# Optimization experiments

Measured on AMD Instinct MI355X. Metric: run time of the kernel, lower is better.

## Reference

```python
import jax, jax.numpy as jnp
import numpy as np

M = 150000  # number of nodes
K = 64      # neighbor_limits[-1]


def setup_inputs() -> dict:
    key = jax.random.key(0)
    k1, k2 = jax.random.split(key)
    nodes = jax.random.normal(k1, (M, 3), dtype=jnp.float32)
    # radius_search-style neighbor table: values in [0, M], where index == M is padding
    node_knn_indices = jax.random.randint(k2, (M, K), 0, M + 1, dtype=jnp.int64)
    return {"nodes": nodes, "node_knn_indices": node_knn_indices}


def _greedy_nms(knn):
    # Sequential greedy suppression: node i is kept iff none of its radius
    # neighbors with smaller index was already kept. masks has size M+1 so the
    # padding index M always reads False (never suppresses).
    m = knn.shape[0]
    masks0 = jnp.zeros(m + 1, dtype=bool)

    def step(masks, xs):
        i, row = xs
        keep = ~jnp.any(masks[row])  # masks[node_knn_indices[i]].sum() == 0
        return masks.at[i].set(keep), None

    masks, _ = jax.lax.scan(step, masks0, (jnp.arange(m), knn))
    return masks


def reference(nodes, node_knn_indices):
    masks = _greedy_nms(node_knn_indices)
    kept = masks[:-1]  # [M] bool
    # Original returns node_knn_indices[kept] (data-dependent shape). For a
    # jit-compatible fixed shape we return the full table with suppressed rows
    # overwritten by the padding index M; kept rows are bitwise identical.
    m = node_knn_indices.shape[0]
    kept_knn = jnp.where(kept[:, None], node_knn_indices, m)
    return kept, kept_knn
```

## Files before the change

### kernel.cpp

```cpp
#include <hip/hip_runtime.h>


#define M_ROWS 150000
#define KNN    64
#define BLK    1024
#define QRT    2
#define CHUNK  (BLK * QRT)
#define NCH    ((M_ROWS + CHUNK - 1) / CHUNK)
#define ICAP   6
#define ECAP   16
#define WCH    8
#define W64PC  (CHUNK / 32)
#define LMW    (((NCH - 1) * CHUNK) / 32)
#define NBMG   ((NCH - 1) * W64PC)
#define OUT_INTS (M_ROWS + M_ROWS * KNN)
#define BMG_INT_OFF (OUT_INTS - NBMG * 2)
#define VALIDB (1ull << 32)

__global__ void init_ws_kernel(unsigned int* progress, int* out) {
  const int i = blockIdx.x * blockDim.x + threadIdx.x;
  unsigned long long* bmg64 = (unsigned long long*)(out + BMG_INT_OFF);
  if (i < NBMG) bmg64[i] = 0ull;
  if (i == 0) *progress = 0u;
}

__device__ __forceinline__ bool probe_reload(const int* __restrict__ rp,
                                             const unsigned int* lm,
                                             int lo, int hi) {
  bool s = false;
#pragma unroll
  for (int u = 0; u < 16; ++u) {
    int4 d = ((const int4*)rp)[u];
    int js[4] = {d.x, d.y, d.z, d.w};
#pragma unroll
    for (int m = 0; m < 4; ++m) {
      int j = js[m];
      if (j >= lo && j < hi && ((lm[j >> 5] >> (j & 31)) & 1u)) s = true;
    }
  }
  return s;
}

__global__ __launch_bounds__(BLK) void nms_chain_kernel(
    const int* __restrict__ knn,
    int* __restrict__ out,
    unsigned int* __restrict__ progress)
{
  const int b    = blockIdx.x;
  const int t    = threadIdx.x;
  const int base = b * CHUNK;
  const int winb = (b > WCH) ? (base - WCH * CHUNK) : 0;

  unsigned long long* bmg64 = (unsigned long long*)(out + BMG_INT_OFF);

  __shared__ unsigned char      st[CHUNK];
  __shared__ unsigned short     il[ICAP][CHUNK];
  __shared__ unsigned short     exl[ECAP][CHUNK];
  __shared__ unsigned int       lm[LMW];
  __shared__ unsigned int       sh_p;

  int  rowq[QRT];
  bool vq[QRT], ovf[QRT], eovf[QRT], supp[QRT];
  int  ic[QRT], ec[QRT];

#pragma unroll
  for (int q = 0; q < QRT; ++q) {
    rowq[q] = base + q * BLK + t;
    vq[q]   = rowq[q] < M_ROWS;
    ic[q] = ec[q] = 0;
    ovf[q] = eovf[q] = supp[q] = false;
  }

#pragma unroll
  for (int q = 0; q < QRT; ++q) {
    if (!vq[q]) continue;
    const int o   = q * BLK + t;
    const int row = rowq[q];
    const int* rp = knn + (long long)row * KNN;
#pragma unroll
    for (int u = 0; u < 16; ++u) {
      int4 d = ((const int4*)rp)[u];
      int js[4] = {d.x, d.y, d.z, d.w};
#pragma unroll
      for (int m = 0; m < 4; ++m) {
        int j = js[m];
        if (j < row) {
          if (j >= base) {
            if (ic[q] < ICAP) il[ic[q]][o] = (unsigned short)(j - base);
            ++ic[q];
          } else if (j >= winb) {
            if (ec[q] < ECAP) exl[ec[q]][o] = (unsigned short)(j - winb);
            ++ec[q];
          }
        }
      }
    }
  }
#pragma unroll
  for (int q = 0; q < QRT; ++q) {
    ovf[q]  = ic[q] > ICAP; if (ovf[q])  ic[q] = ICAP;
    eovf[q] = ec[q] > ECAP; if (eovf[q]) ec[q] = ECAP;
  }

  unsigned short ilr[QRT][ICAP];
#pragma unroll
  for (int q = 0; q < QRT; ++q)
#pragma unroll
    for (int x = 0; x < ICAP; ++x)
      ilr[q][x] = il[x][q * BLK + t];

  int praw1 = 0;
  if (b > WCH) {
    if (t < 64) {
      int pr = 0;
      for (int spin = 0; spin < (1 << 22); ++spin) {
        pr = (int)__hip_atomic_load(progress, __ATOMIC_RELAXED,
                                    __HIP_MEMORY_SCOPE_AGENT);
        if (pr >= b - WCH) break;
        __builtin_amdgcn_s_sleep(2);
      }
      if (t == 0) sh_p = (unsigned int)pr;
    }
    __syncthreads();
    praw1 = (int)sh_p; if (praw1 > b) praw1 = b;
    const int wt = praw1 * W64PC;
    for (int w = t; w < wt; w += BLK) {
      unsigned long long v = __hip_atomic_load(&bmg64[w], __ATOMIC_RELAXED,
                                               __HIP_MEMORY_SCOPE_AGENT);
      int g1 = 0;
      while (!(v & VALIDB) && ++g1 < (1 << 22)) {
        __builtin_amdgcn_s_sleep(1);
        v = __hip_atomic_load(&bmg64[w], __ATOMIC_RELAXED,
                              __HIP_MEMORY_SCOPE_AGENT);
      }
      lm[w] = (unsigned int)v;
    }
    __syncthreads();
    const int lim = praw1 * CHUNK;
#pragma unroll
    for (int q = 0; q < QRT; ++q)
      if (vq[q])
        supp[q] = probe_reload(knn + (long long)rowq[q] * KNN, lm, 0, lim);
  }
  const int pr1lim = praw1 * CHUNK;

  unsigned int extm[QRT];
  bool eunk[QRT];
#pragma unroll
  for (int q = 0; q < QRT; ++q) {
    extm[q] = 0u; eunk[q] = false;
    if (vq[q] && !supp[q]) {
      const int o = q * BLK + t;
      const int n = ec[q];
#pragma unroll
      for (int x = 0; x < ECAP; ++x) {
        if (x < n) {
          const int j = winb + (int)exl[x][o];
          if (j >= pr1lim) extm[q] |= (1u << x);
        }
      }
      eunk[q] = eovf[q];
    }
  }

  unsigned char myst[QRT];
#pragma unroll
  for (int q = 0; q < QRT; ++q) {
    myst[q] = (!vq[q] || supp[q]) ? (unsigned char)2 : (unsigned char)0;
    __hip_atomic_store(&st[q * BLK + t], myst[q],
                       __ATOMIC_RELAXED, __HIP_MEMORY_SCOPE_WORKGROUP);
  }
  __syncthreads();

  bool undec = false;
#pragma unroll
  for (int q = 0; q < QRT; ++q) undec |= (myst[q] == 0);

  for (int pass = 0; pass < (1 << 22) && undec; ++pass) {
    bool pend = false;
    undec = false;
#pragma unroll
    for (int q = 0; q < QRT; ++q) {
      if (myst[q] != 0) continue;
      const int o   = q * BLK + t;
      const int row = base + o;
      bool anyK = false, allD = true;
      unsigned int m = extm[q];

      if (m != 0u) {
#pragma unroll
        for (int g = 0; g < 2; ++g) {
          if ((m >> (g * 8)) & 0xffu) {
            unsigned long long vv[8];
#pragma unroll
            for (int x = 0; x < 8; ++x) {
              const int xe = g * 8 + x;
              const int j = winb + (int)exl[xe][o];
              const int w = ((m >> xe) & 1u) ? (j >> 5) : 0;
              vv[x] = __hip_atomic_load(&bmg64[w], __ATOMIC_RELAXED,
                                        __HIP_MEMORY_SCOPE_AGENT);
            }
#pragma unroll
            for (int x = 0; x < 8; ++x) {
              const int xe = g * 8 + x;
              if ((m >> xe) & 1u) {
                const int j = winb + (int)exl[xe][o];
                if (vv[x] & VALIDB) {
                  if ((vv[x] >> (j & 31)) & 1ull) anyK = true;
                  m &= ~(1u << xe);
                } else pend = true;
              }
            }
          }
        }
        extm[q] = m;
      }

      if (!ovf[q]) {
        unsigned char vsts[ICAP];
#pragma unroll
        for (int x = 0; x < ICAP; ++x) {
          const int ii = (x < ic[q]) ? (int)ilr[q][x] : 0;
          vsts[x] = __hip_atomic_load(&st[ii],
              __ATOMIC_RELAXED, __HIP_MEMORY_SCOPE_WORKGROUP);
        }
#pragma unroll
        for (int x = 0; x < ICAP; ++x) {
          if (x < ic[q]) { anyK |= (vsts[x] == 1); allD &= (vsts[x] != 0); }
        }
      } else {
        const int* rp = knn + (long long)row * KNN;
#pragma unroll
        for (int u = 0; u < 16; ++u) {
          int4 d = ((const int4*)rp)[u];
          int js[4] = {d.x, d.y, d.z, d.w};
          unsigned char sv[4];
#pragma unroll
          for (int m2 = 0; m2 < 4; ++m2) {
            const bool in = (js[m2] >= base && js[m2] < row);
            sv[m2] = __hip_atomic_load(&st[in ? (js[m2] - base) : 0],
                __ATOMIC_RELAXED, __HIP_MEMORY_SCOPE_WORKGROUP);
          }
#pragma unroll
          for (int m2 = 0; m2 < 4; ++m2) {
            if (js[m2] >= base && js[m2] < row) {
              anyK |= (sv[m2] == 1); allD &= (sv[m2] != 0);
            }
          }
        }
      }
      if (extm[q] != 0u) allD = false;

      if (!anyK && eunk[q]) {
        const int lo = (pr1lim > winb) ? pr1lim : winb;
        const int* rp = knn + (long long)row * KNN;
        bool ep = false, ak = false;
#pragma unroll
        for (int g = 0; g < 8; ++g) {
          int js[8];
#pragma unroll
          for (int u = 0; u < 2; ++u) {
            int4 d = ((const int4*)rp)[g * 2 + u];
            js[u * 4 + 0] = d.x; js[u * 4 + 1] = d.y;
            js[u * 4 + 2] = d.z; js[u * 4 + 3] = d.w;
          }
          unsigned long long wv[8];
#pragma unroll
          for (int m2 = 0; m2 < 8; ++m2) {
            const bool in = (js[m2] >= lo && js[m2] < base);
            wv[m2] = __hip_atomic_load(&bmg64[in ? (js[m2] >> 5) : 0],
                __ATOMIC_RELAXED, __HIP_MEMORY_SCOPE_AGENT);
          }
#pragma unroll
          for (int m2 = 0; m2 < 8; ++m2) {
            if (js[m2] >= lo && js[m2] < base) {
              if (wv[m2] & VALIDB) { if ((wv[m2] >> (js[m2] & 31)) & 1ull) ak = true; }
              else ep = true;
            }
          }
        }
        if (ak) anyK = true;
        else if (!ep) eunk[q] = false;
        if (ep) pend = true;
      }
      if (eunk[q]) allD = false;

      if (anyK)      myst[q] = 2;
      else if (allD) myst[q] = 1;
      if (myst[q] != 0)
        __hip_atomic_store(&st[o], myst[q],
                           __ATOMIC_RELAXED, __HIP_MEMORY_SCOPE_WORKGROUP);
      else
        undec = true;
    }
    if (pend) __builtin_amdgcn_s_sleep(1);
  }

  bool kq[QRT];
#pragma unroll
  for (int q = 0; q < QRT; ++q)
    kq[q] = vq[q] && (myst[q] == 1);

  if (b < NCH - 1) {
    const int lane = t & 63;
#pragma unroll
    for (int q = 0; q < QRT; ++q) {
      unsigned long long ba = __ballot(kq[q]);
      const int g = b * W64PC + ((q * BLK + (t & ~63)) >> 5);
      if (lane == 0)
        __hip_atomic_store(&bmg64[g], (ba & 0xffffffffull) | VALIDB,
                           __ATOMIC_RELAXED, __HIP_MEMORY_SCOPE_AGENT);
      if (lane == 32)
        __hip_atomic_store(&bmg64[g + 1], (ba >> 32) | VALIDB,
                           __ATOMIC_RELAXED, __HIP_MEMORY_SCOPE_AGENT);
    }
  }
  __syncthreads();
  if (t == 0)
    __hip_atomic_store(progress, (unsigned int)(b + 1),
                       __ATOMIC_RELAXED, __HIP_MEMORY_SCOPE_AGENT);

#pragma unroll
  for (int q = 0; q < QRT; ++q)
    if (vq[q]) out[rowq[q]] = kq[q] ? 1 : 0;

#pragma unroll
  for (int q = 0; q < QRT; ++q) {
    if (!vq[q]) continue;
    const int row = rowq[q];
    const int* rp = knn + (long long)row * KNN;
    int* orow = out + M_ROWS + (long long)row * KNN;
    const bool k = kq[q];
#pragma unroll
    for (int u = 0; u < 16; ++u) {
      int4 d = ((const int4*)rp)[u];
      int4 o4;
      o4.x = k ? d.x : M_ROWS;
      o4.y = k ? d.y : M_ROWS;
      o4.z = k ? d.z : M_ROWS;
      o4.w = k ? d.w : M_ROWS;
      ((int4*)orow)[u] = o4;
    }
  }
}

extern "C" void kernel_launch(void* const* d_in, const int* in_sizes, int n_in,
                              void* d_out, int out_size, void* d_ws, size_t ws_size,
                              hipStream_t stream) {
  const int* knn = (const int*)d_in[1];
  int* out = (int*)d_out;
  unsigned int* progress = (unsigned int*)d_ws;

  init_ws_kernel<<<(NBMG + BLK - 1) / BLK, BLK, 0, stream>>>(progress, out);
  nms_chain_kernel<<<NCH, BLK, 0, stream>>>(knn, out, progress);
}
```

Baseline: 414.6 us.

## Mirror pending predecessor bitmask words into LDS and publish per-wave early

The LDS bitmask is widened to 64-bit words that carry the valid bit. A single wave polls the not-yet-published predecessor words from global memory and copies them into LDS, so per-row external neighbour checks read LDS instead of issuing agent-scope global atomic loads. Each wave also publishes its kept-bit words as soon as all of its rows are decided, rather than after the whole block finishes. This shortens the chain latency between blocks, but it doubles LDS use for the bitmask and adds a ballot per pass.

```diff
diff --git a/kernel.cpp b/kernel.cpp
--- a/kernel.cpp
+++ b/kernel.cpp
@@ -25,7 +25,7 @@
 }
 
 __device__ __forceinline__ bool probe_reload(const int* __restrict__ rp,
-                                             const unsigned int* lm,
+                                             const unsigned long long* lmq,
                                              int lo, int hi) {
   bool s = false;
 #pragma unroll
@@ -35,7 +35,7 @@
 #pragma unroll
     for (int m = 0; m < 4; ++m) {
       int j = js[m];
-      if (j >= lo && j < hi && ((lm[j >> 5] >> (j & 31)) & 1u)) s = true;
+      if (j >= lo && j < hi && ((lmq[j >> 5] >> (j & 31)) & 1ull)) s = true;
     }
   }
   return s;
@@ -56,7 +56,7 @@
   __shared__ unsigned char      st[CHUNK];
   __shared__ unsigned short     il[ICAP][CHUNK];
   __shared__ unsigned short     exl[ECAP][CHUNK];
-  __shared__ unsigned int       lm[LMW];
+  __shared__ unsigned long long lmq[LMW];
   __shared__ unsigned int       sh_p;
 
   int  rowq[QRT];
@@ -133,16 +133,20 @@
         v = __hip_atomic_load(&bmg64[w], __ATOMIC_RELAXED,
                               __HIP_MEMORY_SCOPE_AGENT);
       }
-      lm[w] = (unsigned int)v;
+      lmq[w] = v;
     }
     __syncthreads();
     const int lim = praw1 * CHUNK;
 #pragma unroll
     for (int q = 0; q < QRT; ++q)
       if (vq[q])
-        supp[q] = probe_reload(knn + (long long)rowq[q] * KNN, lm, 0, lim);
+        supp[q] = probe_reload(knn + (long long)rowq[q] * KNN, lmq, 0, lim);
   }
   const int pr1lim = praw1 * CHUNK;
+  const int ws = praw1 * W64PC;
+  const int we = b * W64PC;
+
+  for (int w = ws + t; w < we; w += BLK) lmq[w] = 0ull;
 
   unsigned int extm[QRT];
   bool eunk[QRT];
@@ -163,6 +167,17 @@
     }
   }
 
+  int wlist[8];
+  unsigned int pw = 0u;
+  if (t < 64) {
+#pragma unroll
+    for (int k = 0; k < 8; ++k) {
+      const int w = ws + t + 64 * k;
+      wlist[k] = (w < we) ? w : 0;
+      if (w < we) pw |= (1u << k);
+    }
+  }
+
   unsigned char myst[QRT];
 #pragma unroll
   for (int q = 0; q < QRT; ++q) {
@@ -175,150 +190,184 @@
   bool undec = false;
 #pragma unroll
   for (int q = 0; q < QRT; ++q) undec |= (myst[q] == 0);
-
-  for (int pass = 0; pass < (1 << 22) && undec; ++pass) {
+  bool pub_done = (b >= NCH - 1);
+
+  for (int pass = 0; pass < (1 << 22); ++pass) {
     bool pend = false;
-    undec = false;
-#pragma unroll
-    for (int q = 0; q < QRT; ++q) {
-      if (myst[q] != 0) continue;
-      const int o   = q * BLK + t;
-      const int row = base + o;
-      bool anyK = false, allD = true;
-      unsigned int m = extm[q];
-
-      if (m != 0u) {
-#pragma unroll
-        for (int g = 0; g < 2; ++g) {
-          if ((m >> (g * 8)) & 0xffu) {
-            unsigned long long vv[8];
-#pragma unroll
-            for (int x = 0; x < 8; ++x) {
-              const int xe = g * 8 + x;
-              const int j = winb + (int)exl[xe][o];
-              const int w = ((m >> xe) & 1u) ? (j >> 5) : 0;
-              vv[x] = __hip_atomic_load(&bmg64[w], __ATOMIC_RELAXED,
-                                        __HIP_MEMORY_SCOPE_AGENT);
-            }
-#pragma unroll
-            for (int x = 0; x < 8; ++x) {
-              const int xe = g * 8 + x;
-              if ((m >> xe) & 1u) {
+
+    if (pw != 0u) {
+      unsigned long long cv[8];
+#pragma unroll
+      for (int k = 0; k < 8; ++k) {
+        const int w = ((pw >> k) & 1u) ? wlist[k] : 0;
+        cv[k] = __hip_atomic_load(&bmg64[w], __ATOMIC_RELAXED,
+                                  __HIP_MEMORY_SCOPE_AGENT);
+      }
+#pragma unroll
+      for (int k = 0; k < 8; ++k) {
+        if ((pw >> k) & 1u) {
+          if (cv[k] & VALIDB) {
+            __hip_atomic_store(&lmq[wlist[k]], cv[k],
+                               __ATOMIC_RELAXED, __HIP_MEMORY_SCOPE_WORKGROUP);
+            pw &= ~(1u << k);
+          } else pend = true;
+        }
+      }
+    }
+
+    if (undec) {
+      undec = false;
+#pragma unroll
+      for (int q = 0; q < QRT; ++q) {
+        if (myst[q] != 0) continue;
+        const int o   = q * BLK + t;
+        const int row = base + o;
+        bool anyK = false, allD = true;
+        unsigned int m = extm[q];
+
+        if (m != 0u) {
+#pragma unroll
+          for (int g = 0; g < 2; ++g) {
+            if ((m >> (g * 8)) & 0xffu) {
+              unsigned long long ev[8];
+#pragma unroll
+              for (int x = 0; x < 8; ++x) {
+                const int xe = g * 8 + x;
                 const int j = winb + (int)exl[xe][o];
-                if (vv[x] & VALIDB) {
-                  if ((vv[x] >> (j & 31)) & 1ull) anyK = true;
-                  m &= ~(1u << xe);
-                } else pend = true;
+                const int w = ((m >> xe) & 1u) ? (j >> 5) : 0;
+                ev[x] = __hip_atomic_load(&lmq[w], __ATOMIC_RELAXED,
+                                          __HIP_MEMORY_SCOPE_WORKGROUP);
               }
-            }
-          }
-        }
-        extm[q] = m;
-      }
-
-      if (!ovf[q]) {
-        unsigned char vsts[ICAP];
-#pragma unroll
-        for (int x = 0; x < ICAP; ++x) {
-          const int ii = (x < ic[q]) ? (int)ilr[q][x] : 0;
-          vsts[x] = __hip_atomic_load(&st[ii],
-              __ATOMIC_RELAXED, __HIP_MEMORY_SCOPE_WORKGROUP);
-        }
-#pragma unroll
-        for (int x = 0; x < ICAP; ++x) {
-          if (x < ic[q]) { anyK |= (vsts[x] == 1); allD &= (vsts[x] != 0); }
-        }
-      } else {
-        const int* rp = knn + (long long)row * KNN;
-#pragma unroll
-        for (int u = 0; u < 16; ++u) {
-          int4 d = ((const int4*)rp)[u];
-          int js[4] = {d.x, d.y, d.z, d.w};
-          unsigned char sv[4];
-#pragma unroll
-          for (int m2 = 0; m2 < 4; ++m2) {
-            const bool in = (js[m2] >= base && js[m2] < row);
-            sv[m2] = __hip_atomic_load(&st[in ? (js[m2] - base) : 0],
+#pragma unroll
+              for (int x = 0; x < 8; ++x) {
+                const int xe = g * 8 + x;
+                if ((m >> xe) & 1u) {
+                  const int j = winb + (int)exl[xe][o];
+                  if (ev[x] & VALIDB) {
+                    if ((ev[x] >> (j & 31)) & 1ull) anyK = true;
+                    m &= ~(1u << xe);
+                  } else pend = true;
+                }
+              }
+            }
+          }
+          extm[q] = m;
+        }
+
+        if (!ovf[q]) {
+          unsigned char vsts[ICAP];
+#pragma unroll
+          for (int x = 0; x < ICAP; ++x) {
+            const int ii = (x < ic[q]) ? (int)ilr[q][x] : 0;
+            vsts[x] = __hip_atomic_load(&st[ii],
                 __ATOMIC_RELAXED, __HIP_MEMORY_SCOPE_WORKGROUP);
           }
 #pragma unroll
-          for (int m2 = 0; m2 < 4; ++m2) {
-            if (js[m2] >= base && js[m2] < row) {
-              anyK |= (sv[m2] == 1); allD &= (sv[m2] != 0);
-            }
-          }
-        }
-      }
-      if (extm[q] != 0u) allD = false;
-
-      if (!anyK && eunk[q]) {
-        const int lo = (pr1lim > winb) ? pr1lim : winb;
-        const int* rp = knn + (long long)row * KNN;
-        bool ep = false, ak = false;
-#pragma unroll
-        for (int g = 0; g < 8; ++g) {
-          int js[8];
-#pragma unroll
-          for (int u = 0; u < 2; ++u) {
-            int4 d = ((const int4*)rp)[g * 2 + u];
-            js[u * 4 + 0] = d.x; js[u * 4 + 1] = d.y;
-            js[u * 4 + 2] = d.z; js[u * 4 + 3] = d.w;
-          }
-          unsigned long long wv[8];
-#pragma unroll
-          for (int m2 = 0; m2 < 8; ++m2) {
-            const bool in = (js[m2] >= lo && js[m2] < base);
-            wv[m2] = __hip_atomic_load(&bmg64[in ? (js[m2] >> 5) : 0],
-                __ATOMIC_RELAXED, __HIP_MEMORY_SCOPE_AGENT);
-          }
-#pragma unroll
-          for (int m2 = 0; m2 < 8; ++m2) {
-            if (js[m2] >= lo && js[m2] < base) {
-              if (wv[m2] & VALIDB) { if ((wv[m2] >> (js[m2] & 31)) & 1ull) ak = true; }
-              else ep = true;
-            }
-          }
-        }
-        if (ak) anyK = true;
-        else if (!ep) eunk[q] = false;
-        if (ep) pend = true;
-      }
-      if (eunk[q]) allD = false;
-
-      if (anyK)      myst[q] = 2;
-      else if (allD) myst[q] = 1;
-      if (myst[q] != 0)
-        __hip_atomic_store(&st[o], myst[q],
-                           __ATOMIC_RELAXED, __HIP_MEMORY_SCOPE_WORKGROUP);
-      else
-        undec = true;
-    }
+          for (int x = 0; x < ICAP; ++x) {
+            if (x < ic[q]) { anyK |= (vsts[x] == 1); allD &= (vsts[x] != 0); }
+          }
+        } else {
+          const int* rp = knn + (long long)row * KNN;
+#pragma unroll
+          for (int u = 0; u < 16; ++u) {
+            int4 d = ((const int4*)rp)[u];
+            int js[4] = {d.x, d.y, d.z, d.w};
+            unsigned char sv[4];
+#pragma unroll
+            for (int m2 = 0; m2 < 4; ++m2) {
+              const bool in = (js[m2] >= base && js[m2] < row);
+              sv[m2] = __hip_atomic_load(&st[in ? (js[m2] - base) : 0],
+                  __ATOMIC_RELAXED, __HIP_MEMORY_SCOPE_WORKGROUP);
+            }
+#pragma unroll
+            for (int m2 = 0; m2 < 4; ++m2) {
+              if (js[m2] >= base && js[m2] < row) {
+                anyK |= (sv[m2] == 1); allD &= (sv[m2] != 0);
+              }
+            }
+          }
+        }
+        if (extm[q] != 0u) allD = false;
+
+        if (!anyK && eunk[q]) {
+          const int lo = (pr1lim > winb) ? pr1lim : winb;
+          const int* rp = knn + (long long)row * KNN;
+          bool ep = false, ak = false;
+#pragma unroll
+          for (int g = 0; g < 8; ++g) {
+            int js[8];
+#pragma unroll
+            for (int u = 0; u < 2; ++u) {
+              int4 d = ((const int4*)rp)[g * 2 + u];
+              js[u * 4 + 0] = d.x; js[u * 4 + 1] = d.y;
+              js[u * 4 + 2] = d.z; js[u * 4 + 3] = d.w;
+            }
+            unsigned long long wv[8];
+#pragma unroll
+            for (int m2 = 0; m2 < 8; ++m2) {
+              const bool in = (js[m2] >= lo && js[m2] < base);
+              wv[m2] = __hip_atomic_load(&lmq[in ? (js[m2] >> 5) : 0],
+                  __ATOMIC_RELAXED, __HIP_MEMORY_SCOPE_WORKGROUP);
+            }
+#pragma unroll
+            for (int m2 = 0; m2 < 8; ++m2) {
+              if (js[m2] >= lo && js[m2] < base) {
+                if (wv[m2] & VALIDB) { if ((wv[m2] >> (js[m2] & 31)) & 1ull) ak = true; }
+                else ep = true;
+              }
+            }
+          }
+          if (ak) anyK = true;
+          else if (!ep) eunk[q] = false;
+          if (ep) pend = true;
+        }
+        if (eunk[q]) allD = false;
+
+        if (anyK)      myst[q] = 2;
+        else if (allD) myst[q] = 1;
+        if (myst[q] != 0)
+          __hip_atomic_store(&st[o], myst[q],
+                             __ATOMIC_RELAXED, __HIP_MEMORY_SCOPE_WORKGROUP);
+        else
+          undec = true;
+      }
+    }
+
+    unsigned long long wdone = __ballot(!undec);
+    if (!pub_done && wdone == ~0ull) {
+      const int lane = t & 63;
+      bool kq0[QRT];
+#pragma unroll
+      for (int q = 0; q < QRT; ++q)
+        kq0[q] = vq[q] && (myst[q] == 1);
+#pragma unroll
+      for (int q = 0; q < QRT; ++q) {
+        unsigned long long ba = __ballot(kq0[q]);
+        const int g = b * W64PC + ((q * BLK + (t & ~63)) >> 5);
+        if (lane == 0)
+          __hip_atomic_store(&bmg64[g], (ba & 0xffffffffull) | VALIDB,
+                             __ATOMIC_RELAXED, __HIP_MEMORY_SCOPE_AGENT);
+        if (lane == 32)
+          __hip_atomic_store(&bmg64[g + 1], (ba >> 32) | VALIDB,
+                             __ATOMIC_RELAXED, __HIP_MEMORY_SCOPE_AGENT);
+      }
+      pub_done = true;
+    }
+
+    const bool mustloop = undec || (pw != 0u);
+    if (__ballot(mustloop) == 0ull) break;
     if (pend) __builtin_amdgcn_s_sleep(1);
   }
 
-  bool kq[QRT];
-#pragma unroll
-  for (int q = 0; q < QRT; ++q)
-    kq[q] = vq[q] && (myst[q] == 1);
-
-  if (b < NCH - 1) {
-    const int lane = t & 63;
-#pragma unroll
-    for (int q = 0; q < QRT; ++q) {
-      unsigned long long ba = __ballot(kq[q]);
-      const int g = b * W64PC + ((q * BLK + (t & ~63)) >> 5);
-      if (lane == 0)
-        __hip_atomic_store(&bmg64[g], (ba & 0xffffffffull) | VALIDB,
-                           __ATOMIC_RELAXED, __HIP_MEMORY_SCOPE_AGENT);
-      if (lane == 32)
-        __hip_atomic_store(&bmg64[g + 1], (ba >> 32) | VALIDB,
-                           __ATOMIC_RELAXED, __HIP_MEMORY_SCOPE_AGENT);
-    }
-  }
   __syncthreads();
   if (t == 0)
     __hip_atomic_store(progress, (unsigned int)(b + 1),
                        __ATOMIC_RELAXED, __HIP_MEMORY_SCOPE_AGENT);
+
+  bool kq[QRT];
+#pragma unroll
+  for (int q = 0; q < QRT; ++q)
+    kq[q] = vq[q] && (myst[q] == 1);
 
 #pragma unroll
   for (int q = 0; q < QRT; ++q)
```

Result: slower. 462.3 us (+11.5%).

## Publish per-row decided bits incrementally so later chunks resolve dependencies early

Applied to the files above, without the earlier changes.

The global bitmap word format changes from a single valid flag to a per-bit decided mask plus a kept mask. Each wavefront republishes its decided and kept ballots whenever its decided set changes during the resolution loop, rather than once at the end. Rows with no in-chunk or external dependencies are marked kept up front, and extra intra-chunk sweeps are added per pass. Later blocks can therefore consume partial results from earlier chunks and shorten the cross-block serial dependency chain. The cost is more global atomic stores and ballots per pass, and the block-wide waits must now see every decided bit set before they proceed.

```diff
diff --git a/kernel.cpp b/kernel.cpp
--- a/kernel.cpp
+++ b/kernel.cpp
@@ -15,7 +15,7 @@
 #define NBMG   ((NCH - 1) * W64PC)
 #define OUT_INTS (M_ROWS + M_ROWS * KNN)
 #define BMG_INT_OFF (OUT_INTS - NBMG * 2)
-#define VALIDB (1ull << 32)
+#define DECFULL 0xffffffffu
 
 __global__ void init_ws_kernel(unsigned int* progress, int* out) {
   const int i = blockIdx.x * blockDim.x + threadIdx.x;
@@ -128,7 +128,7 @@
       unsigned long long v = __hip_atomic_load(&bmg64[w], __ATOMIC_RELAXED,
                                                __HIP_MEMORY_SCOPE_AGENT);
       int g1 = 0;
-      while (!(v & VALIDB) && ++g1 < (1 << 22)) {
+      while (((unsigned int)(v >> 32)) != DECFULL && ++g1 < (1 << 22)) {
         __builtin_amdgcn_s_sleep(1);
         v = __hip_atomic_load(&bmg64[w], __ATOMIC_RELAXED,
                               __HIP_MEMORY_SCOPE_AGENT);
@@ -166,159 +166,224 @@
   unsigned char myst[QRT];
 #pragma unroll
   for (int q = 0; q < QRT; ++q) {
-    myst[q] = (!vq[q] || supp[q]) ? (unsigned char)2 : (unsigned char)0;
+    myst[q] = (!vq[q] || supp[q]) ? (unsigned char)2
+            : ((ic[q] == 0 && !ovf[q] && extm[q] == 0u && !eunk[q])
+               ? (unsigned char)1 : (unsigned char)0);
     __hip_atomic_store(&st[q * BLK + t], myst[q],
                        __ATOMIC_RELAXED, __HIP_MEMORY_SCOPE_WORKGROUP);
   }
   __syncthreads();
 
-  bool undec = false;
-#pragma unroll
-  for (int q = 0; q < QRT; ++q) undec |= (myst[q] == 0);
-
-  for (int pass = 0; pass < (1 << 22) && undec; ++pass) {
-    bool pend = false;
-    undec = false;
+  const int lane = t & 63;
+  unsigned long long lastd[QRT];
+#pragma unroll
+  for (int q = 0; q < QRT; ++q) lastd[q] = 0ull;
+  if (b < NCH - 1) {
 #pragma unroll
     for (int q = 0; q < QRT; ++q) {
-      if (myst[q] != 0) continue;
-      const int o   = q * BLK + t;
-      const int row = base + o;
-      bool anyK = false, allD = true;
-      unsigned int m = extm[q];
-
-      if (m != 0u) {
-#pragma unroll
-        for (int g = 0; g < 2; ++g) {
-          if ((m >> (g * 8)) & 0xffu) {
-            unsigned long long vv[8];
-#pragma unroll
-            for (int x = 0; x < 8; ++x) {
-              const int xe = g * 8 + x;
-              const int j = winb + (int)exl[xe][o];
-              const int w = ((m >> xe) & 1u) ? (j >> 5) : 0;
-              vv[x] = __hip_atomic_load(&bmg64[w], __ATOMIC_RELAXED,
-                                        __HIP_MEMORY_SCOPE_AGENT);
-            }
-#pragma unroll
-            for (int x = 0; x < 8; ++x) {
-              const int xe = g * 8 + x;
-              if ((m >> xe) & 1u) {
-                const int j = winb + (int)exl[xe][o];
-                if (vv[x] & VALIDB) {
-                  if ((vv[x] >> (j & 31)) & 1ull) anyK = true;
-                  m &= ~(1u << xe);
-                } else pend = true;
-              }
-            }
-          }
-        }
-        extm[q] = m;
-      }
-
-      if (!ovf[q]) {
-        unsigned char vsts[ICAP];
-#pragma unroll
-        for (int x = 0; x < ICAP; ++x) {
-          const int ii = (x < ic[q]) ? (int)ilr[q][x] : 0;
-          vsts[x] = __hip_atomic_load(&st[ii],
-              __ATOMIC_RELAXED, __HIP_MEMORY_SCOPE_WORKGROUP);
-        }
-#pragma unroll
-        for (int x = 0; x < ICAP; ++x) {
-          if (x < ic[q]) { anyK |= (vsts[x] == 1); allD &= (vsts[x] != 0); }
-        }
-      } else {
-        const int* rp = knn + (long long)row * KNN;
-#pragma unroll
-        for (int u = 0; u < 16; ++u) {
-          int4 d = ((const int4*)rp)[u];
-          int js[4] = {d.x, d.y, d.z, d.w};
-          unsigned char sv[4];
-#pragma unroll
-          for (int m2 = 0; m2 < 4; ++m2) {
-            const bool in = (js[m2] >= base && js[m2] < row);
-            sv[m2] = __hip_atomic_load(&st[in ? (js[m2] - base) : 0],
-                __ATOMIC_RELAXED, __HIP_MEMORY_SCOPE_WORKGROUP);
-          }
-#pragma unroll
-          for (int m2 = 0; m2 < 4; ++m2) {
-            if (js[m2] >= base && js[m2] < row) {
-              anyK |= (sv[m2] == 1); allD &= (sv[m2] != 0);
-            }
-          }
-        }
-      }
-      if (extm[q] != 0u) allD = false;
-
-      if (!anyK && eunk[q]) {
-        const int lo = (pr1lim > winb) ? pr1lim : winb;
-        const int* rp = knn + (long long)row * KNN;
-        bool ep = false, ak = false;
-#pragma unroll
-        for (int g = 0; g < 8; ++g) {
-          int js[8];
-#pragma unroll
-          for (int u = 0; u < 2; ++u) {
-            int4 d = ((const int4*)rp)[g * 2 + u];
-            js[u * 4 + 0] = d.x; js[u * 4 + 1] = d.y;
-            js[u * 4 + 2] = d.z; js[u * 4 + 3] = d.w;
-          }
-          unsigned long long wv[8];
-#pragma unroll
-          for (int m2 = 0; m2 < 8; ++m2) {
-            const bool in = (js[m2] >= lo && js[m2] < base);
-            wv[m2] = __hip_atomic_load(&bmg64[in ? (js[m2] >> 5) : 0],
-                __ATOMIC_RELAXED, __HIP_MEMORY_SCOPE_AGENT);
-          }
-#pragma unroll
-          for (int m2 = 0; m2 < 8; ++m2) {
-            if (js[m2] >= lo && js[m2] < base) {
-              if (wv[m2] & VALIDB) { if ((wv[m2] >> (js[m2] & 31)) & 1ull) ak = true; }
-              else ep = true;
-            }
-          }
-        }
-        if (ak) anyK = true;
-        else if (!ep) eunk[q] = false;
-        if (ep) pend = true;
-      }
-      if (eunk[q]) allD = false;
-
-      if (anyK)      myst[q] = 2;
-      else if (allD) myst[q] = 1;
-      if (myst[q] != 0)
-        __hip_atomic_store(&st[o], myst[q],
-                           __ATOMIC_RELAXED, __HIP_MEMORY_SCOPE_WORKGROUP);
-      else
-        undec = true;
-    }
-    if (pend) __builtin_amdgcn_s_sleep(1);
-  }
-
-  bool kq[QRT];
-#pragma unroll
-  for (int q = 0; q < QRT; ++q)
-    kq[q] = vq[q] && (myst[q] == 1);
-
-  if (b < NCH - 1) {
-    const int lane = t & 63;
-#pragma unroll
-    for (int q = 0; q < QRT; ++q) {
-      unsigned long long ba = __ballot(kq[q]);
+      unsigned long long bdec  = __ballot(myst[q] != 0);
+      unsigned long long bkept = __ballot(myst[q] == 1);
       const int g = b * W64PC + ((q * BLK + (t & ~63)) >> 5);
       if (lane == 0)
-        __hip_atomic_store(&bmg64[g], (ba & 0xffffffffull) | VALIDB,
-                           __ATOMIC_RELAXED, __HIP_MEMORY_SCOPE_AGENT);
+        __hip_atomic_store(&bmg64[g],
+            ((bdec & 0xffffffffull) << 32) | (bkept & 0xffffffffull),
+            __ATOMIC_RELAXED, __HIP_MEMORY_SCOPE_AGENT);
       if (lane == 32)
-        __hip_atomic_store(&bmg64[g + 1], (ba >> 32) | VALIDB,
-                           __ATOMIC_RELAXED, __HIP_MEMORY_SCOPE_AGENT);
-    }
-  }
+        __hip_atomic_store(&bmg64[g + 1],
+            ((bdec >> 32) << 32) | (bkept >> 32),
+            __ATOMIC_RELAXED, __HIP_MEMORY_SCOPE_AGENT);
+      lastd[q] = bdec;
+    }
+  }
+
+  bool undec = false;
+#pragma unroll
+  for (int q = 0; q < QRT; ++q) undec |= (myst[q] == 0);
+
+  for (int pass = 0; pass < (1 << 22); ++pass) {
+    bool pend = false;
+    if (undec) {
+#pragma unroll
+      for (int q = 0; q < QRT; ++q) {
+        if (myst[q] != 0) continue;
+        const int o   = q * BLK + t;
+        const int row = base + o;
+        bool anyK = false, allD = true;
+        unsigned int m = extm[q];
+
+        if (m != 0u) {
+#pragma unroll
+          for (int g = 0; g < 2; ++g) {
+            if ((m >> (g * 8)) & 0xffu) {
+              unsigned long long vv[8];
+#pragma unroll
+              for (int x = 0; x < 8; ++x) {
+                const int xe = g * 8 + x;
+                const int j = winb + (int)exl[xe][o];
+                const int w = ((m >> xe) & 1u) ? (j >> 5) : 0;
+                vv[x] = __hip_atomic_load(&bmg64[w], __ATOMIC_RELAXED,
+                                          __HIP_MEMORY_SCOPE_AGENT);
+              }
+#pragma unroll
+              for (int x = 0; x < 8; ++x) {
+                const int xe = g * 8 + x;
+                if ((m >> xe) & 1u) {
+                  const int j = winb + (int)exl[xe][o];
+                  const int bit = j & 31;
+                  if ((((unsigned int)(vv[x] >> 32)) >> bit) & 1u) {
+                    if ((((unsigned int)vv[x]) >> bit) & 1u) anyK = true;
+                    m &= ~(1u << xe);
+                  } else pend = true;
+                }
+              }
+            }
+          }
+          extm[q] = m;
+        }
+
+        if (!ovf[q]) {
+          unsigned char vsts[ICAP];
+#pragma unroll
+          for (int x = 0; x < ICAP; ++x) {
+            const int ii = (x < ic[q]) ? (int)ilr[q][x] : 0;
+            vsts[x] = __hip_atomic_load(&st[ii],
+                __ATOMIC_RELAXED, __HIP_MEMORY_SCOPE_WORKGROUP);
+          }
+#pragma unroll
+          for (int x = 0; x < ICAP; ++x) {
+            if (x < ic[q]) { anyK |= (vsts[x] == 1); allD &= (vsts[x] != 0); }
+          }
+        } else {
+          const int* rp = knn + (long long)row * KNN;
+#pragma unroll
+          for (int u = 0; u < 16; ++u) {
+            int4 d = ((const int4*)rp)[u];
+            int js[4] = {d.x, d.y, d.z, d.w};
+            unsigned char sv[4];
+#pragma unroll
+            for (int m2 = 0; m2 < 4; ++m2) {
+              const bool in = (js[m2] >= base && js[m2] < row);
+              sv[m2] = __hip_atomic_load(&st[in ? (js[m2] - base) : 0],
+                  __ATOMIC_RELAXED, __HIP_MEMORY_SCOPE_WORKGROUP);
+            }
+#pragma unroll
+            for (int m2 = 0; m2 < 4; ++m2) {
+              if (js[m2] >= base && js[m2] < row) {
+                anyK |= (sv[m2] == 1); allD &= (sv[m2] != 0);
+              }
+            }
+          }
+        }
+        if (extm[q] != 0u) allD = false;
+
+        if (!anyK && eunk[q]) {
+          const int lo = (pr1lim > winb) ? pr1lim : winb;
+          const int* rp = knn + (long long)row * KNN;
+          bool ep = false, ak = false;
+#pragma unroll
+          for (int g = 0; g < 8; ++g) {
+            int js[8];
+#pragma unroll
+            for (int u = 0; u < 2; ++u) {
+              int4 d = ((const int4*)rp)[g * 2 + u];
+              js[u * 4 + 0] = d.x; js[u * 4 + 1] = d.y;
+              js[u * 4 + 2] = d.z; js[u * 4 + 3] = d.w;
+            }
+            unsigned long long wv[8];
+#pragma unroll
+            for (int m2 = 0; m2 < 8; ++m2) {
+              const bool in = (js[m2] >= lo && js[m2] < base);
+              wv[m2] = __hip_atomic_load(&bmg64[in ? (js[m2] >> 5) : 0],
+                  __ATOMIC_RELAXED, __HIP_MEMORY_SCOPE_AGENT);
+            }
+#pragma unroll
+            for (int m2 = 0; m2 < 8; ++m2) {
+              if (js[m2] >= lo && js[m2] < base) {
+                const int bit = js[m2] & 31;
+                if ((((unsigned int)(wv[m2] >> 32)) >> bit) & 1u) {
+                  if ((((unsigned int)wv[m2]) >> bit) & 1u) ak = true;
+                } else ep = true;
+              }
+            }
+          }
+          if (ak) anyK = true;
+          else if (!ep) eunk[q] = false;
+          if (ep) pend = true;
+        }
+        if (eunk[q]) allD = false;
+
+        if (anyK)      myst[q] = 2;
+        else if (allD) myst[q] = 1;
+        if (myst[q] != 0)
+          __hip_atomic_store(&st[o], myst[q],
+                             __ATOMIC_RELAXED, __HIP_MEMORY_SCOPE_WORKGROUP);
+      }
+
+#pragma unroll
+      for (int s = 0; s < 2; ++s) {
+#pragma unroll
+        for (int q = 0; q < QRT; ++q) {
+          if (myst[q] != 0 || ovf[q]) continue;
+          const int o = q * BLK + t;
+          bool anyK = false, allD = true;
+          unsigned char vsts[ICAP];
+#pragma unroll
+          for (int x = 0; x < ICAP; ++x) {
+            const int ii = (x < ic[q]) ? (int)ilr[q][x] : 0;
+            vsts[x] = __hip_atomic_load(&st[ii],
+                __ATOMIC_RELAXED, __HIP_MEMORY_SCOPE_WORKGROUP);
+          }
+#pragma unroll
+          for (int x = 0; x < ICAP; ++x) {
+            if (x < ic[q]) { anyK |= (vsts[x] == 1); allD &= (vsts[x] != 0); }
+          }
+          if (extm[q] != 0u || eunk[q]) allD = false;
+          if (anyK)      myst[q] = 2;
+          else if (allD) myst[q] = 1;
+          if (myst[q] != 0)
+            __hip_atomic_store(&st[o], myst[q],
+                               __ATOMIC_RELAXED, __HIP_MEMORY_SCOPE_WORKGROUP);
+        }
+      }
+
+      undec = false;
+#pragma unroll
+      for (int q = 0; q < QRT; ++q) undec |= (myst[q] == 0);
+    }
+
+    if (b < NCH - 1) {
+#pragma unroll
+      for (int q = 0; q < QRT; ++q) {
+        unsigned long long bdec = __ballot(myst[q] != 0);
+        if (bdec != lastd[q]) {
+          unsigned long long bkept = __ballot(myst[q] == 1);
+          const int g = b * W64PC + ((q * BLK + (t & ~63)) >> 5);
+          if (lane == 0)
+            __hip_atomic_store(&bmg64[g],
+                ((bdec & 0xffffffffull) << 32) | (bkept & 0xffffffffull),
+                __ATOMIC_RELAXED, __HIP_MEMORY_SCOPE_AGENT);
+          if (lane == 32)
+            __hip_atomic_store(&bmg64[g + 1],
+                ((bdec >> 32) << 32) | (bkept >> 32),
+                __ATOMIC_RELAXED, __HIP_MEMORY_SCOPE_AGENT);
+          lastd[q] = bdec;
+        }
+      }
+    }
+
+    if (__ballot(undec) == 0ull) break;
+    if (__ballot(pend) != 0ull) __builtin_amdgcn_s_sleep(1);
+  }
+
   __syncthreads();
   if (t == 0)
     __hip_atomic_store(progress, (unsigned int)(b + 1),
                        __ATOMIC_RELAXED, __HIP_MEMORY_SCOPE_AGENT);
+
+  bool kq[QRT];
+#pragma unroll
+  for (int q = 0; q < QRT; ++q)
+    kq[q] = vq[q] && (myst[q] == 1);
 
 #pragma unroll
   for (int q = 0; q < QRT; ++q)
```

After: 376.0 us. 1.1x faster.
